# Performance work log

Hardware: AMD Instinct MI355X
Metric: run time of the kernel (lower is better)

The kernel has to match this reference:

```python
import jax, jax.numpy as jnp
import numpy as np


def setup_inputs() -> dict:
    key = jax.random.key(0)
    k1, k2 = jax.random.split(key)
    x = jax.random.normal(k1, (8, 2048, 1024), dtype=jnp.float32)
    codebooks = jax.random.normal(k2, (8, 2048, 128), dtype=jnp.float32)
    return {"x": x, "codebooks": codebooks}


def reference(x, codebooks):
    # x: [b, n, h*d]; codebooks: [h, m, d]
    b, n, f = x.shape
    h, m, d = codebooks.shape
    q = x.reshape(b, n, h, d).transpose(0, 2, 1, 3)  # [b, h, n, d]
    # squared L2 distance: ||q||^2 + ||c||^2 - 2 q.c
    l2_q = jnp.sum(q * q, axis=-1, keepdims=True)          # [b, h, n, 1]
    l2_c = jnp.sum(codebooks * codebooks, axis=-1)          # [h, m]
    sim = jnp.einsum('bhnd,hmd->bhnm', q, codebooks)        # [b, h, n, m]
    dist = l2_q + l2_c[None, :, None, :] - 2.0 * sim
    idx = jnp.argmin(dist, axis=-1)                          # [b, h, n]
    # direct gather instead of one-hot @ codebook (same math)
    quant = codebooks[jnp.arange(h)[None, :, None], idx]     # [b, h, n, d]
    quant = quant.transpose(0, 2, 1, 3).reshape(b, n, f)
    # straight-through estimator (training-mode forward)
    out = x + jax.lax.stop_gradient(quant - x)
    return out
```

## Files before the change

kernel.cpp:

```cpp
#include <hip/hip_runtime.h>
#include <stddef.h>
#include <stdint.h>


#define NHEAD  8
#define NCODE  2048
#define DDIM   128
#define NQTOT  16384
#define BQ     128
#define CCH    64
#define NCHUNK (NCODE / CCH)
#define CHB    (CCH * DDIM * 2)
#define TAU    0.05f
#define WS_NEED (4u*1024u*1024u + 64u*1024u)

typedef __attribute__((ext_vector_type(8))) _Float16 half8;
typedef __attribute__((ext_vector_type(4))) float f32x4;

__global__ __launch_bounds__(256) void vq_prep(const float* __restrict__ cb,
                                               unsigned char* __restrict__ ws)
{
  _Float16* img = (_Float16*)ws;
  float* cn = (float*)(ws + 4u*1024u*1024u);

  const int tg   = blockIdx.x * 256 + threadIdx.x;
  const int rg   = tg >> 4;
  const int slot = tg & 15;
  const int m    = rg & (NCODE - 1);
  const int rowc = m & 63;
  const int srcslot = slot ^ (rowc & 7);

  const float* src = cb + (size_t)rg * DDIM + srcslot * 8;
  float4 a = *(const float4*)(src);
  float4 b = *(const float4*)(src + 4);
  float f[8] = {a.x, a.y, a.z, a.w, b.x, b.y, b.z, b.w};
  half8 hv;
  float nrm = 0.f;
#pragma unroll
  for (int j = 0; j < 8; ++j) {
    float v = f[j];
    nrm = fmaf(v, v, nrm);
    hv[j] = (_Float16)v;
  }
  size_t off = ((size_t)(rg >> 6) * 16384 + rowc * 256 + slot * 16) / 2;
  *(half8*)(img + off) = hv;
#pragma unroll
  for (int msk = 1; msk < 16; msk <<= 1) nrm += __shfl_xor(nrm, msk);
  if (slot == 0) cn[rg] = 0.5f * nrm;
}

__global__ __launch_bounds__(256) void vq_main(const float* __restrict__ x,
                                               const float* __restrict__ cb,
                                               const unsigned char* __restrict__ ws,
                                               float* __restrict__ out)
{
  __shared__ __align__(16) unsigned char Ct[2][CHB];
  __shared__ int   fidx[BQ];
  __shared__ int   flaglist[BQ];
  __shared__ int   nflag;
  __shared__ float qrow[DDIM];
  __shared__ float redS[4];
  __shared__ int   redI[4];

  const int tid  = threadIdx.x;
  const int w    = tid >> 6, l = tid & 63;
  const int lrow = l & 15,  lg = l >> 4;
  const int h    = blockIdx.y;
  const int qbase = blockIdx.x * BQ;

  const unsigned char* img = ws;
  const float* cnh = (const float*)(ws + 4u*1024u*1024u) + h * NCODE;
  const float* cbh = cb + (size_t)h * NCODE * DDIM;

  if (tid == 0) nflag = 0;

  half8 Ah[2][4], Al[2][4];
#pragma unroll
  for (int rf = 0; rf < 2; ++rf)
#pragma unroll
    for (int ks = 0; ks < 4; ++ks) {
      const float* p = x + (size_t)(qbase + w*32 + rf*16 + lrow) * 1024
                         + h * DDIM + ks * 32 + lg * 8;
      float4 a = *(const float4*)p;
      float4 b = *(const float4*)(p + 4);
      float f[8] = {a.x, a.y, a.z, a.w, b.x, b.y, b.z, b.w};
#pragma unroll
      for (int j = 0; j < 8; ++j) {
        _Float16 hh = (_Float16)f[j];
        Ah[rf][ks][j] = hh;
        Al[rf][ks][j] = (_Float16)(f[j] - (float)hh);
      }
    }

  float best[8], sec[8];
  int   bidx[8];
#pragma unroll
  for (int i = 0; i < 8; ++i) { best[i] = 3.4e38f; sec[i] = 3.4e38f; bidx[i] = 0; }

  const size_t himgbase = (size_t)h * 32 * 16384;
  auto STAGE = [&](int buf, int c) {
    const unsigned char* g = img + himgbase + (size_t)c * 16384;
    unsigned char* lb = &Ct[buf][0];
#pragma unroll
    for (int r = 0; r < 4; ++r) {
      const int sub = (r * 4 + w) * 1024;
      __builtin_amdgcn_global_load_lds(
          (const __attribute__((address_space(1))) void*)(g + sub + l * 16),
          (__attribute__((address_space(3))) void*)(lb + sub), 16, 0, 0);
    }
  };

  STAGE(0, 0);
  __syncthreads();

  int cur = 0;
  for (int c = 0; c < NCHUNK; ++c) {
    if (c + 1 < NCHUNK) STAGE(cur ^ 1, c + 1);

    const int cbase = c * CCH;
    float cnv[4];
#pragma unroll
    for (int cf = 0; cf < 4; ++cf) cnv[cf] = cnh[cbase + cf * 16 + lrow];

    f32x4 acc[2][4];
#pragma unroll
    for (int rf = 0; rf < 2; ++rf)
#pragma unroll
      for (int cf = 0; cf < 4; ++cf) acc[rf][cf] = (f32x4){0.f, 0.f, 0.f, 0.f};

    const unsigned char* lb = &Ct[cur][0];
#pragma unroll
    for (int ks = 0; ks < 4; ++ks) {
#pragma unroll
      for (int cf = 0; cf < 4; ++cf) {
        const int row  = cf * 16 + lrow;
        const int boff = row * 256 + (((ks * 4 + lg) ^ (row & 7)) * 16);
        half8 bh = *(const half8*)(lb + boff);
#pragma unroll
        for (int rf = 0; rf < 2; ++rf) {
          acc[rf][cf] = __builtin_amdgcn_mfma_f32_16x16x32_f16(Ah[rf][ks], bh, acc[rf][cf], 0, 0, 0);
          acc[rf][cf] = __builtin_amdgcn_mfma_f32_16x16x32_f16(Al[rf][ks], bh, acc[rf][cf], 0, 0, 0);
        }
      }
    }

#pragma unroll
    for (int cf = 0; cf < 4; ++cf) {
      const int m0 = cbase + cf * 16 + lrow;
#pragma unroll
      for (int rf = 0; rf < 2; ++rf)
#pragma unroll
        for (int r = 0; r < 4; ++r) {
          const float s = cnv[cf] - acc[rf][cf][r];
          const int sl = rf * 4 + r;
          if (s < best[sl]) { sec[sl] = best[sl]; best[sl] = s; bidx[sl] = m0; }
          else               sec[sl] = fminf(sec[sl], s);
        }
    }
    __syncthreads();
    cur ^= 1;
  }

#pragma unroll
  for (int msk = 1; msk < 16; msk <<= 1) {
#pragma unroll
    for (int sl = 0; sl < 8; ++sl) {
      float ob = __shfl_xor(best[sl], msk);
      float os = __shfl_xor(sec[sl],  msk);
      int   oi = __shfl_xor(bidx[sl], msk);
      bool owin = (ob < best[sl]) || (ob == best[sl] && oi < bidx[sl]);
      float lose = owin ? best[sl] : ob;
      best[sl] = owin ? ob : best[sl];
      bidx[sl] = owin ? oi : bidx[sl];
      sec[sl]  = fminf(fminf(sec[sl], os), lose);
    }
  }
  if (lrow == 0) {
#pragma unroll
    for (int sl = 0; sl < 8; ++sl) {
      const int rf = sl >> 2, r = sl & 3;
      const int qloc = w * 32 + rf * 16 + lg * 4 + r;
      fidx[qloc] = bidx[sl];
      if (sec[sl] - best[sl] < TAU) {
        int p = atomicAdd(&nflag, 1);
        flaglist[p] = qloc;
      }
    }
  }
  __syncthreads();

  const int nf = nflag;
  for (int fi = 0; fi < nf; ++fi) {
    const int qloc = flaglist[fi];
    if (tid < DDIM) qrow[tid] = x[(size_t)(qbase + qloc) * 1024 + h * DDIM + tid];
    __syncthreads();
    float bs = 3.4e38f; int bi = NCODE;
    for (int m = tid; m < NCODE; m += 256) {
      const float* cp = cbh + (size_t)m * DDIM;
      float dot = 0.f;
#pragma unroll
      for (int d = 0; d < DDIM; d += 4) {
        float4 c4 = *(const float4*)(cp + d);
        dot = fmaf(qrow[d + 0], c4.x, dot);
        dot = fmaf(qrow[d + 1], c4.y, dot);
        dot = fmaf(qrow[d + 2], c4.z, dot);
        dot = fmaf(qrow[d + 3], c4.w, dot);
      }
      const float s = cnh[m] - dot;
      if (s < bs) { bs = s; bi = m; }
    }
#pragma unroll
    for (int msk = 1; msk < 64; msk <<= 1) {
      float ob = __shfl_xor(bs, msk);
      int   oi = __shfl_xor(bi, msk);
      if (ob < bs || (ob == bs && oi < bi)) { bs = ob; bi = oi; }
    }
    if (l == 0) { redS[w] = bs; redI[w] = bi; }
    __syncthreads();
    if (tid == 0) {
      float fb = redS[0]; int fbi = redI[0];
      for (int ww = 1; ww < 4; ++ww)
        if (redS[ww] < fb || (redS[ww] == fb && redI[ww] < fbi)) { fb = redS[ww]; fbi = redI[ww]; }
      fidx[qloc] = fbi;
    }
    __syncthreads();
  }

  const int half = tid >> 7, lane = tid & 127;
  for (int r = half; r < BQ; r += 2) {
    const int m = fidx[r];
    out[(size_t)(qbase + r) * 1024 + h * DDIM + lane] = cbh[(size_t)m * DDIM + lane];
  }
}

#define FBQ  128
#define FNCH 128
#define FDK  32
#define FLDP 132

__global__ __launch_bounds__(256) void vq_argmin_fallback(
    const float* __restrict__ x, const float* __restrict__ cb, float* __restrict__ out)
{
  __shared__ float Qs[FDK][FLDP];
  __shared__ float Cs[FDK][FLDP];
  __shared__ float cnc[FNCH];
  __shared__ float redS[FBQ][16];
  __shared__ int   redI[FBQ][16];
  __shared__ int   fidx[FBQ];

  const int h = blockIdx.y, qbase = blockIdx.x * FBQ, tid = threadIdx.x;
  const int ty = tid >> 4, tx = tid & 15;
  const float* xh  = x + (size_t)qbase * 1024 + (size_t)h * DDIM;
  const float* cbh = cb + (size_t)h * NCODE * DDIM;

  float best[8]; int bidx[8];
#pragma unroll
  for (int i = 0; i < 8; ++i) { best[i] = 3.4e38f; bidx[i] = 0; }
  float acc[8][8];
#pragma unroll
  for (int i = 0; i < 8; ++i)
#pragma unroll
    for (int j = 0; j < 8; ++j) acc[i][j] = 0.f;

  const int r0 = tid >> 3, c4 = tid & 7;
  for (int mc = 0; mc < NCODE / FNCH; ++mc) {
    for (int dk = 0; dk < DDIM / FDK; ++dk) {
      __syncthreads();
#pragma unroll
      for (int p = 0; p < 4; ++p) {
        const int q = p * 32 + r0;
        float4 v = *(const float4*)(xh + (size_t)q * 1024 + dk * FDK + c4 * 4);
        Qs[c4*4+0][q] = v.x; Qs[c4*4+1][q] = v.y; Qs[c4*4+2][q] = v.z; Qs[c4*4+3][q] = v.w;
        float4 wv = *(const float4*)(cbh + (size_t)(mc*FNCH + q) * DDIM + dk * FDK + c4 * 4);
        Cs[c4*4+0][q] = wv.x; Cs[c4*4+1][q] = wv.y; Cs[c4*4+2][q] = wv.z; Cs[c4*4+3][q] = wv.w;
      }
      __syncthreads();
#pragma unroll 8
      for (int d = 0; d < FDK; ++d) {
        float4 qa = *(const float4*)&Qs[d][ty*8];
        float4 qb = *(const float4*)&Qs[d][ty*8+4];
        float4 ca = *(const float4*)&Cs[d][tx*8];
        float4 cb4 = *(const float4*)&Cs[d][tx*8+4];
        const float qv[8] = {qa.x,qa.y,qa.z,qa.w,qb.x,qb.y,qb.z,qb.w};
        const float cv[8] = {ca.x,ca.y,ca.z,ca.w,cb4.x,cb4.y,cb4.z,cb4.w};
#pragma unroll
        for (int i = 0; i < 8; ++i)
#pragma unroll
          for (int j = 0; j < 8; ++j) acc[i][j] = fmaf(qv[i], cv[j], acc[i][j]);
      }
      if (tid < FNCH) {
        float s = 0.f;
#pragma unroll
        for (int d = 0; d < FDK; ++d) { float v = Cs[d][tid]; s = fmaf(v, v, s); }
        if (dk == 0) cnc[tid] = s; else cnc[tid] += s;
      }
    }
    __syncthreads();
#pragma unroll
    for (int j = 0; j < 8; ++j) {
      const int ml = tx * 8 + j;
      const float cn = 0.5f * cnc[ml];
      const int mg = mc * FNCH + ml;
#pragma unroll
      for (int i = 0; i < 8; ++i) {
        const float s = cn - acc[i][j];
        if (s < best[i]) { best[i] = s; bidx[i] = mg; }
        acc[i][j] = 0.f;
      }
    }
  }
#pragma unroll
  for (int i = 0; i < 8; ++i) { redS[ty*8+i][tx] = best[i]; redI[ty*8+i][tx] = bidx[i]; }
  __syncthreads();
  if (tid < FBQ) {
    float bs = redS[tid][0]; int bi = redI[tid][0];
#pragma unroll
    for (int t = 1; t < 16; ++t) {
      const float s = redS[tid][t]; const int ii = redI[tid][t];
      if (s < bs || (s == bs && ii < bi)) { bs = s; bi = ii; }
    }
    fidx[tid] = bi;
  }
  __syncthreads();
  const int half = tid >> 7, lane = tid & 127;
  for (int r = half; r < FBQ; r += 2) {
    const int m = fidx[r];
    out[(size_t)(qbase + r) * 1024 + (size_t)h * DDIM + lane] = cbh[(size_t)m * DDIM + lane];
  }
}

extern "C" void kernel_launch(void* const* d_in, const int* in_sizes, int n_in,
                              void* d_out, int out_size, void* d_ws, size_t ws_size,
                              hipStream_t stream)
{
  const float* x   = (const float*)d_in[0];
  const float* cbk = (const float*)d_in[1];
  float*       out = (float*)d_out;

  if (ws_size >= (size_t)WS_NEED) {
    vq_prep<<<dim3(1024), dim3(256), 0, stream>>>(cbk, (unsigned char*)d_ws);
    vq_main<<<dim3(NQTOT / BQ, NHEAD), dim3(256), 0, stream>>>(
        x, cbk, (const unsigned char*)d_ws, out);
  } else {
    vq_argmin_fallback<<<dim3(NQTOT / FBQ, NHEAD), dim3(256), 0, stream>>>(x, cbk, out);
  }
}
```

Baseline: 612.6 us.

## Triple-buffer codebook chunks with norms packed into LDS staging

```diff
diff --git a/kernel.cpp b/kernel.cpp
--- a/kernel.cpp
+++ b/kernel.cpp
@@ -10,9 +10,10 @@
 #define BQ     128
 #define CCH    64
 #define NCHUNK (NCODE / CCH)
-#define CHB    (CCH * DDIM * 2)
+#define CHB2   16640
 #define TAU    0.05f
-#define WS_NEED (4u*1024u*1024u + 64u*1024u)
+#define CN_OFF (8u * 32u * 16640u)
+#define WS_NEED (CN_OFF + 16384u * 4u)
 
 typedef __attribute__((ext_vector_type(8))) _Float16 half8;
 typedef __attribute__((ext_vector_type(4))) float f32x4;
@@ -20,14 +21,10 @@
 __global__ __launch_bounds__(256) void vq_prep(const float* __restrict__ cb,
                                                unsigned char* __restrict__ ws)
 {
-  _Float16* img = (_Float16*)ws;
-  float* cn = (float*)(ws + 4u*1024u*1024u);
-
   const int tg   = blockIdx.x * 256 + threadIdx.x;
   const int rg   = tg >> 4;
   const int slot = tg & 15;
-  const int m    = rg & (NCODE - 1);
-  const int rowc = m & 63;
+  const int rowc = rg & 63;
   const int srcslot = slot ^ (rowc & 7);
 
   const float* src = cb + (size_t)rg * DDIM + srcslot * 8;
@@ -42,11 +39,14 @@
     nrm = fmaf(v, v, nrm);
     hv[j] = (_Float16)v;
   }
-  size_t off = ((size_t)(rg >> 6) * 16384 + rowc * 256 + slot * 16) / 2;
-  *(half8*)(img + off) = hv;
+  *(half8*)(ws + (size_t)(rg >> 6) * CHB2 + rowc * 256 + slot * 16) = hv;
 #pragma unroll
   for (int msk = 1; msk < 16; msk <<= 1) nrm += __shfl_xor(nrm, msk);
-  if (slot == 0) cn[rg] = 0.5f * nrm;
+  if (slot == 0) {
+    const float v = 0.5f * nrm;
+    *(float*)(ws + (size_t)(rg >> 6) * CHB2 + 16384 + rowc * 4) = v;
+    ((float*)(ws + CN_OFF))[rg] = v;
+  }
 }
 
 __global__ __launch_bounds__(256) void vq_main(const float* __restrict__ x,
@@ -54,7 +54,7 @@
                                                const unsigned char* __restrict__ ws,
                                                float* __restrict__ out)
 {
-  __shared__ __align__(16) unsigned char Ct[2][CHB];
+  __shared__ __align__(256) unsigned char Ct[3 * CHB2];
   __shared__ int   fidx[BQ];
   __shared__ int   flaglist[BQ];
   __shared__ int   nflag;
@@ -65,11 +65,11 @@
   const int tid  = threadIdx.x;
   const int w    = tid >> 6, l = tid & 63;
   const int lrow = l & 15,  lg = l >> 4;
-  const int h    = blockIdx.y;
-  const int qbase = blockIdx.x * BQ;
+  const int h     = blockIdx.x & 7;
+  const int qbase = (blockIdx.x >> 3) * BQ;
 
   const unsigned char* img = ws;
-  const float* cnh = (const float*)(ws + 4u*1024u*1024u) + h * NCODE;
+  const float* cnh = (const float*)(ws + CN_OFF) + h * NCODE;
   const float* cbh = cb + (size_t)h * NCODE * DDIM;
 
   if (tid == 0) nflag = 0;
@@ -97,10 +97,10 @@
 #pragma unroll
   for (int i = 0; i < 8; ++i) { best[i] = 3.4e38f; sec[i] = 3.4e38f; bidx[i] = 0; }
 
-  const size_t himgbase = (size_t)h * 32 * 16384;
+  const size_t himgbase = (size_t)h * 32 * CHB2;
   auto STAGE = [&](int buf, int c) {
-    const unsigned char* g = img + himgbase + (size_t)c * 16384;
-    unsigned char* lb = &Ct[buf][0];
+    const unsigned char* g = img + himgbase + (size_t)c * CHB2;
+    unsigned char* lb = &Ct[buf * CHB2];
 #pragma unroll
     for (int r = 0; r < 4; ++r) {
       const int sub = (r * 4 + w) * 1024;
@@ -108,19 +108,24 @@
           (const __attribute__((address_space(1))) void*)(g + sub + l * 16),
           (__attribute__((address_space(3))) void*)(lb + sub), 16, 0, 0);
     }
+    __builtin_amdgcn_global_load_lds(
+        (const __attribute__((address_space(1))) void*)(g + 16384 + l * 4),
+        (__attribute__((address_space(3))) void*)(lb + 16384), 4, 0, 0);
   };
 
-  STAGE(0, 0);
-  __syncthreads();
-
-  int cur = 0;
+  STAGE(0, 0); STAGE(1, 1); STAGE(2, 2);
+
+  int bufc = 0;
   for (int c = 0; c < NCHUNK; ++c) {
-    if (c + 1 < NCHUNK) STAGE(cur ^ 1, c + 1);
-
+    asm volatile("s_waitcnt vmcnt(10)" ::: "memory");
+    __builtin_amdgcn_s_barrier();
+
+    const unsigned char* lb = &Ct[bufc * CHB2];
     const int cbase = c * CCH;
     float cnv[4];
 #pragma unroll
-    for (int cf = 0; cf < 4; ++cf) cnv[cf] = cnh[cbase + cf * 16 + lrow];
+    for (int cf = 0; cf < 4; ++cf)
+      cnv[cf] = *(const float*)(lb + 16384 + (cf * 16 + lrow) * 4);
 
     f32x4 acc[2][4];
 #pragma unroll
@@ -128,7 +133,6 @@
 #pragma unroll
       for (int cf = 0; cf < 4; ++cf) acc[rf][cf] = (f32x4){0.f, 0.f, 0.f, 0.f};
 
-    const unsigned char* lb = &Ct[cur][0];
 #pragma unroll
     for (int ks = 0; ks < 4; ++ks) {
 #pragma unroll
@@ -157,9 +161,12 @@
           else               sec[sl] = fminf(sec[sl], s);
         }
     }
-    __syncthreads();
-    cur ^= 1;
-  }
+
+    __builtin_amdgcn_s_barrier();
+    STAGE(bufc, (c + 3) & (NCHUNK - 1));
+    bufc = (bufc == 2) ? 0 : bufc + 1;
+  }
+  __syncthreads();
 
 #pragma unroll
   for (int msk = 1; msk < 16; msk <<= 1) {
@@ -339,7 +346,7 @@
 
   if (ws_size >= (size_t)WS_NEED) {
     vq_prep<<<dim3(1024), dim3(256), 0, stream>>>(cbk, (unsigned char*)d_ws);
-    vq_main<<<dim3(NQTOT / BQ, NHEAD), dim3(256), 0, stream>>>(
+    vq_main<<<dim3(NQTOT / BQ * NHEAD), dim3(256), 0, stream>>>(
         x, cbk, (const unsigned char*)d_ws, out);
   } else {
     vq_argmin_fallback<<<dim3(NQTOT / FBQ, NHEAD), dim3(256), 0, stream>>>(x, cbk, out);
```

After: 618.2 us. About the same (+0.9%).
